# Performance work log

Hardware: AMD Instinct MI355X
Metric: run time of the kernel (lower is better)

The kernel has to match this reference:

```python
import jax, jax.numpy as jnp
import numpy as np

NEG_SLOPE = 0.2
EPS = 1e-16

def gat_layer(x, W, a_src, a_dst, bias, src, dst, N, H, C):
    # x: [N, F_in]; W: [F_in, H*C]; a_src/a_dst: [H, C]; bias: [H*C]
    h = (x @ W).reshape(N, H, C)                       # [N,H,C]
    alpha_src = (h * a_src[None]).sum(-1)              # [N,H]
    alpha_dst = (h * a_dst[None]).sum(-1)              # [N,H]
    e = jax.nn.leaky_relu(alpha_src[src] + alpha_dst[dst], NEG_SLOPE)  # [E,H]
    m = jax.ops.segment_max(e, dst, num_segments=N)    # [N,H]
    ex = jnp.exp(e - m[dst])
    s = jax.ops.segment_sum(ex, dst, num_segments=N)   # [N,H]
    alpha = ex / (s[dst] + EPS)                        # [E,H]
    out = jax.ops.segment_sum(h[src] * alpha[:, :, None], dst, num_segments=N)  # [N,H,C]
    return out.reshape(N, H * C) + bias

def setup_inputs() -> dict:
    key = jax.random.key(0)
    ks = jax.random.split(key, 12)
    N, E, Ep = 50000, 800000, 100000
    Fin, Hd, Co, H = 128, 128, 64, 2
    x = jax.random.normal(ks[0], (N, Fin), jnp.float32)
    edge_index = jax.random.randint(ks[1], (2, E), 0, N, jnp.int64)
    pos_edge_index = jax.random.randint(ks[2], (2, Ep), 0, N, jnp.int64)
    W1 = jax.random.normal(ks[3], (Fin, H * Hd), jnp.float32) / np.sqrt(Fin)
    a1_src = jax.random.normal(ks[4], (H, Hd), jnp.float32) / np.sqrt(Hd)
    a1_dst = jax.random.normal(ks[5], (H, Hd), jnp.float32) / np.sqrt(Hd)
    b1 = jnp.zeros((H * Hd,), jnp.float32)
    W2 = jax.random.normal(ks[6], (H * Hd, H * Co), jnp.float32) / np.sqrt(H * Hd)
    a2_src = jax.random.normal(ks[7], (H, Co), jnp.float32) / np.sqrt(Co)
    a2_dst = jax.random.normal(ks[8], (H, Co), jnp.float32) / np.sqrt(Co)
    b2 = jnp.zeros((H * Co,), jnp.float32)
    return {"x": x, "edge_index": edge_index, "pos_edge_index": pos_edge_index,
            "W1": W1, "a1_src": a1_src, "a1_dst": a1_dst, "b1": b1,
            "W2": W2, "a2_src": a2_src, "a2_dst": a2_dst, "b2": b2}

def reference(x, edge_index, pos_edge_index, W1, a1_src, a1_dst, b1, W2, a2_src, a2_dst, b2):
    N = x.shape[0]
    H = a1_src.shape[0]
    # add self loops (PyG GATConv default)
    loop = jnp.arange(N, dtype=edge_index.dtype)
    src = jnp.concatenate([edge_index[0], loop])
    dst = jnp.concatenate([edge_index[1], loop])
    h1 = gat_layer(x, W1, a1_src, a1_dst, b1, src, dst, N, H, a1_src.shape[1])
    h1 = jax.nn.relu(h1)  # dropout is identity in eval mode
    z = gat_layer(h1, W2, a2_src, a2_dst, b2, src, dst, N, H, a2_src.shape[1])
    # decode: dot product per positive edge
    return (z[pos_edge_index[0]] * z[pos_edge_index[1]]).sum(-1)
```

## Files before the change

### kernel.cpp

```cpp
#include <hip/hip_runtime.h>

#define NEG_SLOPE 0.2f
#define EPS_F 1e-16f
#define STILE 4096

typedef short short8 __attribute__((ext_vector_type(8)));
typedef float f32x4 __attribute__((ext_vector_type(4)));

__device__ __forceinline__ unsigned short f2bf(float x) {
    unsigned u = __float_as_uint(x);
    return (unsigned short)((u + 0x7FFFu + ((u >> 16) & 1u)) >> 16);
}
__device__ __forceinline__ float bflo(unsigned q) { return __uint_as_float(q << 16); }
__device__ __forceinline__ float bfhi(unsigned q) { return __uint_as_float(q & 0xFFFF0000u); }


template<int MB, int K, typename TIN>
__device__ __forceinline__ void gemm_body(
        const TIN* __restrict__ X, const unsigned short* __restrict__ Wt,
        unsigned short* __restrict__ Y, float* __restrict__ as_out,
        float* __restrict__ ad_out, const float* __restrict__ a_srcf,
        const float* __restrict__ a_dstf, int N, int bid,
        unsigned short* lds) {
    constexpr int NT_ = MB / 16;
    constexpr int C   = MB / 2;
    constexpr int KS  = K / 32;
    constexpr int KP  = K + 8;
    int tid  = threadIdx.x;
    int w    = tid >> 6, lane = tid & 63;
    int li   = lane & 15, kc = lane >> 4;
    int n0   = bid * 64 + w * 16;
    int arow = min(n0 + li, N - 1);

    constexpr int CHUNKS = MB * K / 8;
#pragma unroll
    for (int c = 0; c < CHUNKS / 256; ++c) {
        int id = tid + c * 256;
        int m = id / (K / 8), k8 = id % (K / 8);
        *(uint4*)&lds[m * KP + k8 * 8] = *(const uint4*)&Wt[m * K + k8 * 8];
    }
    short8 a[KS];
#pragma unroll
    for (int ks = 0; ks < KS; ++ks) {
        if constexpr (sizeof(TIN) == 4) {
            const float* xp = (const float*)X + (size_t)arow * K + ks * 32 + kc * 8;
            float4 xa = *(const float4*)xp;
            float4 xb = *(const float4*)(xp + 4);
            a[ks][0] = (short)f2bf(xa.x); a[ks][1] = (short)f2bf(xa.y);
            a[ks][2] = (short)f2bf(xa.z); a[ks][3] = (short)f2bf(xa.w);
            a[ks][4] = (short)f2bf(xb.x); a[ks][5] = (short)f2bf(xb.y);
            a[ks][6] = (short)f2bf(xb.z); a[ks][7] = (short)f2bf(xb.w);
        } else {
            a[ks] = *(const short8*)((const unsigned short*)X + (size_t)arow * K + ks * 32 + kc * 8);
        }
    }
    __syncthreads();

    f32x4 acc[NT_];
#pragma unroll
    for (int ct = 0; ct < NT_; ++ct) acc[ct] = (f32x4){0.f, 0.f, 0.f, 0.f};
#pragma unroll
    for (int ct = 0; ct < NT_; ++ct) {
        const unsigned short* wb = lds + (ct * 16 + li) * KP + kc * 8;
#pragma unroll
        for (int ks = 0; ks < KS; ++ks) {
            short8 b = *(const short8*)(wb + ks * 32);
            acc[ct] = __builtin_amdgcn_mfma_f32_16x16x32_bf16(a[ks], b, acc[ct], 0, 0, 0);
        }
    }

    float av[NT_], dv[NT_];
#pragma unroll
    for (int ct = 0; ct < NT_; ++ct) {
        av[ct] = a_srcf[ct * 16 + li];
        dv[ct] = a_dstf[ct * 16 + li];
    }
    int row_base = n0 + kc * 4;
#pragma unroll
    for (int r = 0; r < 4; ++r) {
        int n = row_base + r;
        float vs0 = 0.f, vs1 = 0.f, vd0 = 0.f, vd1 = 0.f;
#pragma unroll
        for (int ct = 0; ct < NT_; ++ct) {
            float v = acc[ct][r];
            if (ct * 16 < C) { vs0 = fmaf(v, av[ct], vs0); vd0 = fmaf(v, dv[ct], vd0); }
            else             { vs1 = fmaf(v, av[ct], vs1); vd1 = fmaf(v, dv[ct], vd1); }
        }
#pragma unroll
        for (int off = 1; off < 16; off <<= 1) {
            vs0 += __shfl_xor(vs0, off);
            vs1 += __shfl_xor(vs1, off);
            vd0 += __shfl_xor(vd0, off);
            vd1 += __shfl_xor(vd1, off);
        }
        if (n < N) {
            if (li == 0) {
                as_out[n * 2] = vs0; as_out[n * 2 + 1] = vs1;
                ad_out[n * 2] = vd0; ad_out[n * 2 + 1] = vd1;
            }
#pragma unroll
            for (int ct = 0; ct < NT_; ++ct)
                Y[(size_t)n * MB + ct * 16 + li] = f2bf(acc[ct][r]);
        }
    }
}

__device__ __forceinline__ void scan_part_body(const int* __restrict__ deg,
                                               int* __restrict__ tsum, int b) {
    __shared__ int wsh[4];
    int t = threadIdx.x;
    int base = b * STILE + t * 16;
    int sum = 0;
#pragma unroll
    for (int j = 0; j < 16; j += 4) {
        int4 q = *(const int4*)&deg[base + j];
        sum += q.x + q.y + q.z + q.w;
    }
#pragma unroll
    for (int off = 32; off; off >>= 1) sum += __shfl_down(sum, off);
    if ((t & 63) == 0) wsh[t >> 6] = sum;
    __syncthreads();
    if (t == 0) tsum[b] = wsh[0] + wsh[1] + wsh[2] + wsh[3];
}


__global__ void k_prep_hist(const float* __restrict__ W1, unsigned short* __restrict__ Wt1,
                            int K1, int M1,
                            const float* __restrict__ W2, unsigned short* __restrict__ Wt2,
                            int K2, int M2, int nPrepBlk,
                            const int* __restrict__ ei, int E, int N,
                            int* __restrict__ deg) {
    if ((int)blockIdx.x < nPrepBlk) {
        int i = blockIdx.x * 256 + threadIdx.x;
        int n1 = M1 * K1;
        if (i < n1) {
            int m = i / K1, k = i - m * K1;
            Wt1[i] = f2bf(W1[(size_t)k * M1 + m]);
        } else {
            int j = i - n1;
            if (j < M2 * K2) {
                int m = j / K2, k = j - m * K2;
                Wt2[j] = f2bf(W2[(size_t)k * M2 + m]);
            }
        }
    } else {
        int e = (blockIdx.x - nPrepBlk) * 256 + threadIdx.x;
        if (e >= E + N) return;
        int d = (e < E) ? ei[E + e] : e - E;
        atomicAdd(&deg[d], 1);
    }
}

__global__ __launch_bounds__(256) void k_gemm1_scan(
        const float* __restrict__ X, const unsigned short* __restrict__ Wt,
        unsigned short* __restrict__ Y, float* __restrict__ as_out,
        float* __restrict__ ad_out, const float* __restrict__ a_srcf,
        const float* __restrict__ a_dstf, int N, int GB,
        const int* __restrict__ deg, int* __restrict__ tsum) {
    __shared__ __align__(16) unsigned short lds[256 * (128 + 8)];
    if ((int)blockIdx.x < GB)
        gemm_body<256, 128, float>(X, Wt, Y, as_out, ad_out, a_srcf, a_dstf, N,
                                   blockIdx.x, lds);
    else
        scan_part_body(deg, tsum, blockIdx.x - GB);
}

__global__ __launch_bounds__(256) void k_gemm2(
        const unsigned short* __restrict__ X, const unsigned short* __restrict__ Wt,
        unsigned short* __restrict__ Y, float* __restrict__ as_out,
        float* __restrict__ ad_out, const float* __restrict__ a_srcf,
        const float* __restrict__ a_dstf, int N) {
    __shared__ __align__(16) unsigned short lds[128 * (256 + 8)];
    gemm_body<128, 256, unsigned short>(X, Wt, Y, as_out, ad_out, a_srcf, a_dstf, N,
                                        blockIdx.x, lds);
}

__global__ __launch_bounds__(256) void scan_final(const int* __restrict__ deg,
                                                  const int* __restrict__ tsum,
                                                  int* __restrict__ rowptr,
                                                  int* __restrict__ cursor) {
    int b = blockIdx.x, t = threadIdx.x, lane = t & 63, wid = t >> 6;
    int base = b * STILE + t * 16;
    int tpre = 0;
    for (int j = 0; j < b; ++j) tpre += tsum[j];
    int v[16];
    int sum = 0;
#pragma unroll
    for (int j = 0; j < 16; j += 4) {
        int4 q = *(const int4*)&deg[base + j];
        v[j] = q.x; v[j + 1] = q.y; v[j + 2] = q.z; v[j + 3] = q.w;
        sum += q.x + q.y + q.z + q.w;
    }
    int x = sum;
#pragma unroll
    for (int off = 1; off < 64; off <<= 1) {
        int y = __shfl_up(x, off);
        if (lane >= off) x += y;
    }
    __shared__ int wtot[4];
    if (lane == 63) wtot[wid] = x;
    __syncthreads();
    int woff = 0;
    for (int wi = 0; wi < wid; ++wi) woff += wtot[wi];
    int run = tpre + woff + (x - sum);
    int outv[16];
#pragma unroll
    for (int j = 0; j < 16; ++j) { outv[j] = run; run += v[j]; }
#pragma unroll
    for (int j = 0; j < 16; j += 4) {
        *(int4*)&rowptr[base + j] = make_int4(outv[j], outv[j+1], outv[j+2], outv[j+3]);
        *(int4*)&cursor[base + j] = make_int4(0, 0, 0, 0);
    }
}

__global__ void fill_kernel(const int* __restrict__ ei, int E, int N,
                            const int* __restrict__ rowptr, int* __restrict__ cursor,
                            int* __restrict__ csr_src) {
    int e = blockIdx.x * blockDim.x + threadIdx.x;
    if (e >= E + N) return;
    int s, d;
    if (e < E) { s = ei[e]; d = ei[E + e]; } else { s = d = e - E; }
    int pos = atomicAdd(&cursor[d], 1);
    csr_src[rowptr[d] + pos] = s;
}

template<int M, int C, typename TOUT>
__global__ __launch_bounds__(256) void fused_attn_agg(
        const int* __restrict__ rowptr, const int* __restrict__ csr_src,
        const float* __restrict__ as_, const float* __restrict__ ad_,
        const unsigned short* __restrict__ hfeat, const float* __restrict__ bias,
        TOUT* __restrict__ outp, int N, int do_relu) {
    constexpr int VEC = M / 64;
    __shared__ __align__(16) uint2 pb0[4][64];
    __shared__ __align__(16) uint2 pb1[4][64];
    int n    = (blockIdx.x * blockDim.x + threadIdx.x) >> 6;
    int lane = threadIdx.x & 63;
    int w    = (threadIdx.x >> 6) & 3;
    if (n >= N) return;
    int cbase = lane * VEC;
    int hh    = cbase / C;
    int r0 = rowptr[n], r1 = rowptr[n + 1];
    const float2* as2 = (const float2*)as_;
    float2 adv = ((const float2*)ad_)[n];
    float sa0 = 0.f, sa1 = 0.f;
    float acc[VEC];
#pragma unroll
    for (int v = 0; v < VEC; ++v) acc[v] = 0.f;
    const uint2* ap = (hh == 0) ? pb0[w] : pb1[w];

    for (int base = r0; base < r1; base += 64) {
        int cnt = min(64, r1 - base);
        int srcl = 0;
        float sc0 = -INFINITY, sc1 = -INFINITY;
        if (lane < cnt) {
            srcl = csr_src[base + lane];
            float2 asv = as2[srcl];
            float e0 = asv.x + adv.x;
            float e1 = asv.y + adv.y;
            sc0 = (e0 > 0.f) ? e0 : NEG_SLOPE * e0;
            sc1 = (e1 > 0.f) ? e1 : NEG_SLOPE * e1;
        }
        float p0 = expf(sc0), p1 = expf(sc1);
        sa0 += p0; sa1 += p1;
        unsigned off = (unsigned)srcl * (M * 2);
        pb0[w][lane] = make_uint2(off, __float_as_uint(p0));
        pb1[w][lane] = make_uint2(off, __float_as_uint(p1));
        for (int e = 0; e < cnt; e += 2) {
            uint4 qq = *(const uint4*)&ap[e];
            float pa = __uint_as_float(qq.y);
            float pc = __uint_as_float(qq.w);
            const unsigned short* hp0 = (const unsigned short*)((const char*)hfeat + qq.x) + cbase;
            const unsigned short* hp1 = (const unsigned short*)((const char*)hfeat + qq.z) + cbase;
            if constexpr (VEC == 4) {
                uint2 g0 = *(const uint2*)hp0;
                uint2 g1 = *(const uint2*)hp1;
                acc[0] += pa * bflo(g0.x); acc[1] += pa * bfhi(g0.x);
                acc[2] += pa * bflo(g0.y); acc[3] += pa * bfhi(g0.y);
                acc[0] += pc * bflo(g1.x); acc[1] += pc * bfhi(g1.x);
                acc[2] += pc * bflo(g1.y); acc[3] += pc * bfhi(g1.y);
            } else {
                unsigned g0 = *(const unsigned*)hp0;
                unsigned g1 = *(const unsigned*)hp1;
                acc[0] += pa * bflo(g0); acc[1] += pa * bfhi(g0);
                acc[0] += pc * bflo(g1); acc[1] += pc * bfhi(g1);
            }
        }
    }
#pragma unroll
    for (int off = 32; off; off >>= 1) {
        sa0 += __shfl_xor(sa0, off);
        sa1 += __shfl_xor(sa1, off);
    }
    float ssum = (hh == 0) ? sa0 : sa1;
    float inv = 1.f / (ssum + EPS_F);
    float o[VEC];
#pragma unroll
    for (int v = 0; v < VEC; ++v) {
        float val = acc[v] * inv + bias[cbase + v];
        o[v] = do_relu ? fmaxf(val, 0.f) : val;
    }
    if constexpr (sizeof(TOUT) == 2) {
        unsigned short* op = (unsigned short*)outp + (size_t)n * M + cbase;
        if constexpr (VEC == 4) {
            uint2 pk;
            pk.x = (unsigned)f2bf(o[0]) | ((unsigned)f2bf(o[1]) << 16);
            pk.y = (unsigned)f2bf(o[2]) | ((unsigned)f2bf(o[3]) << 16);
            *(uint2*)op = pk;
        } else {
            *(unsigned*)op = (unsigned)f2bf(o[0]) | ((unsigned)f2bf(o[1]) << 16);
        }
    } else {
        float* op = (float*)outp + (size_t)n * M + cbase;
        if constexpr (VEC == 4) *(float4*)op = make_float4(o[0], o[1], o[2], o[3]);
        else                    *(float2*)op = make_float2(o[0], o[1]);
    }
}

__global__ void decode_kernel(const int* __restrict__ pei, int Ep,
                              const float* __restrict__ z, int D,
                              float* __restrict__ out) {
    int wid  = (blockIdx.x * blockDim.x + threadIdx.x) >> 6;
    int lane = threadIdx.x & 63;
    if (wid >= Ep) return;
    int a = pei[wid], b = pei[Ep + wid];
    const float2* za = (const float2*)(z + (size_t)a * D);
    const float2* zb = (const float2*)(z + (size_t)b * D);
    float s = 0.f;
    for (int i = lane; i < D / 2; i += 64) {
        float2 xv = za[i], yv = zb[i];
        s += xv.x * yv.x + xv.y * yv.y;
    }
    for (int off = 32; off; off >>= 1) s += __shfl_down(s, off);
    if (lane == 0) out[wid] = s;
}

extern "C" void kernel_launch(void* const* d_in, const int* in_sizes, int n_in,
                              void* d_out, int out_size, void* d_ws, size_t ws_size,
                              hipStream_t stream) {
    const float* x   = (const float*)d_in[0];
    const int*   ei  = (const int*)d_in[1];
    const int*   pei = (const int*)d_in[2];
    const float* W1  = (const float*)d_in[3];
    const float* a1s = (const float*)d_in[4];
    const float* a1d = (const float*)d_in[5];
    const float* b1  = (const float*)d_in[6];
    const float* W2  = (const float*)d_in[7];
    const float* a2s = (const float*)d_in[8];
    const float* a2d = (const float*)d_in[9];
    const float* b2  = (const float*)d_in[10];
    float* out = (float*)d_out;

    const int M1  = in_sizes[6];
    const int Fin = in_sizes[3] / M1;
    const int N   = in_sizes[0] / Fin;
    const int E   = in_sizes[1] / 2;
    const int Ep  = in_sizes[2] / 2;
    const int M2  = in_sizes[10];
    const int Etot = E + N;
    const int NT  = (N + STILE - 1) / STILE;

    unsigned short* hbf  = (unsigned short*)d_ws;
    unsigned short* h1bf = hbf + (size_t)N * M1;
    float* zbuf    = (float*)(h1bf + (size_t)N * M1);
    float* as_     = zbuf + (size_t)N * M2;
    float* ad_     = as_ + (size_t)N * 2;
    int*   deg     = (int*)(ad_ + (size_t)N * 2);
    int*   rowptr  = deg + (size_t)NT * STILE;
    int*   cursor  = rowptr + (size_t)NT * STILE;
    int*   tsum    = cursor + (size_t)NT * STILE;
    int*   csr_src = tsum + 64;
    unsigned short* wt1 = (unsigned short*)(csr_src + Etot);
    unsigned short* wt2 = wt1 + (size_t)M1 * Fin;

    dim3 blk256(256);

    hipMemsetAsync(deg, 0, (size_t)NT * STILE * sizeof(int), stream);

    int nPrepBlk = (M1 * Fin + M2 * M1 + 255) / 256;
    int nHistBlk = (Etot + 255) / 256;
    k_prep_hist<<<nPrepBlk + nHistBlk, blk256, 0, stream>>>(
        W1, wt1, Fin, M1, W2, wt2, M1, M2, nPrepBlk, ei, E, N, deg);

    int GB = (N + 63) / 64;
    k_gemm1_scan<<<GB + NT, blk256, 0, stream>>>(
        x, wt1, hbf, as_, ad_, a1s, a1d, N, GB, deg, tsum);

    scan_final<<<NT, blk256, 0, stream>>>(deg, tsum, rowptr, cursor);
    fill_kernel<<<nHistBlk, blk256, 0, stream>>>(ei, E, N, rowptr, cursor, csr_src);

    fused_attn_agg<256, 128, unsigned short><<<(N + 3) / 4, blk256, 0, stream>>>(
        rowptr, csr_src, as_, ad_, hbf, b1, h1bf, N, 1);

    k_gemm2<<<(N + 63) / 64, blk256, 0, stream>>>(
        h1bf, wt2, hbf, as_, ad_, a2s, a2d, N);

    fused_attn_agg<128, 64, float><<<(N + 3) / 4, blk256, 0, stream>>>(
        rowptr, csr_src, as_, ad_, hbf, b2, zbuf, N, 0);

    decode_kernel<<<(Ep * 64 + 255) / 256, blk256, 0, stream>>>(
        pei, Ep, zbuf, M2, out);
}
```

Measured before the change: 254.5 us.

## Fuse CSR fill into gemm1, store z as bf16, halve decode wave work

Moves the scan before the first GEMM so the CSR fill can run as extra blocks in the same launch as gemm1, overlapping atomic scatter with matrix work. The layer-2 output z is now stored in bf16, and decode processes two edges per wavefront with 32 lanes each, reading packed bf16 pairs. Hidden-feature pointer arithmetic in the aggregation loop is simplified by hoisting the column offset. The bf16 z adds rounding error to the final dot products, and the scan kernels now run as standalone small launches.

```diff
diff --git a/kernel.cpp b/kernel.cpp
--- a/kernel.cpp
+++ b/kernel.cpp
@@ -121,6 +121,18 @@
     if ((t & 63) == 0) wsh[t >> 6] = sum;
     __syncthreads();
     if (t == 0) tsum[b] = wsh[0] + wsh[1] + wsh[2] + wsh[3];
+}
+
+__device__ __forceinline__ void fill_body(const int* __restrict__ ei, int E, int N,
+                                          const int* __restrict__ rowptr,
+                                          int* __restrict__ cursor,
+                                          int* __restrict__ csr_src, int bid) {
+    int e = bid * 256 + threadIdx.x;
+    if (e >= E + N) return;
+    int s, d;
+    if (e < E) { s = ei[e]; d = ei[E + e]; } else { s = d = e - E; }
+    int pos = atomicAdd(&cursor[d], 1);
+    csr_src[rowptr[d] + pos] = s;
 }
 
 
@@ -151,28 +163,9 @@
     }
 }
 
-__global__ __launch_bounds__(256) void k_gemm1_scan(
-        const float* __restrict__ X, const unsigned short* __restrict__ Wt,
-        unsigned short* __restrict__ Y, float* __restrict__ as_out,
-        float* __restrict__ ad_out, const float* __restrict__ a_srcf,
-        const float* __restrict__ a_dstf, int N, int GB,
-        const int* __restrict__ deg, int* __restrict__ tsum) {
-    __shared__ __align__(16) unsigned short lds[256 * (128 + 8)];
-    if ((int)blockIdx.x < GB)
-        gemm_body<256, 128, float>(X, Wt, Y, as_out, ad_out, a_srcf, a_dstf, N,
-                                   blockIdx.x, lds);
-    else
-        scan_part_body(deg, tsum, blockIdx.x - GB);
-}
-
-__global__ __launch_bounds__(256) void k_gemm2(
-        const unsigned short* __restrict__ X, const unsigned short* __restrict__ Wt,
-        unsigned short* __restrict__ Y, float* __restrict__ as_out,
-        float* __restrict__ ad_out, const float* __restrict__ a_srcf,
-        const float* __restrict__ a_dstf, int N) {
-    __shared__ __align__(16) unsigned short lds[128 * (256 + 8)];
-    gemm_body<128, 256, unsigned short>(X, Wt, Y, as_out, ad_out, a_srcf, a_dstf, N,
-                                        blockIdx.x, lds);
+__global__ __launch_bounds__(256) void k_scan_part(const int* __restrict__ deg,
+                                                   int* __restrict__ tsum) {
+    scan_part_body(deg, tsum, blockIdx.x);
 }
 
 __global__ __launch_bounds__(256) void scan_final(const int* __restrict__ deg,
@@ -213,15 +206,30 @@
     }
 }
 
-__global__ void fill_kernel(const int* __restrict__ ei, int E, int N,
-                            const int* __restrict__ rowptr, int* __restrict__ cursor,
-                            int* __restrict__ csr_src) {
-    int e = blockIdx.x * blockDim.x + threadIdx.x;
-    if (e >= E + N) return;
-    int s, d;
-    if (e < E) { s = ei[e]; d = ei[E + e]; } else { s = d = e - E; }
-    int pos = atomicAdd(&cursor[d], 1);
-    csr_src[rowptr[d] + pos] = s;
+__global__ __launch_bounds__(256) void k_gemm1_fill(
+        const float* __restrict__ X, const unsigned short* __restrict__ Wt,
+        unsigned short* __restrict__ Y, float* __restrict__ as_out,
+        float* __restrict__ ad_out, const float* __restrict__ a_srcf,
+        const float* __restrict__ a_dstf, int N, int GB,
+        const int* __restrict__ ei, int E,
+        const int* __restrict__ rowptr, int* __restrict__ cursor,
+        int* __restrict__ csr_src) {
+    __shared__ __align__(16) unsigned short lds[256 * (128 + 8)];
+    if ((int)blockIdx.x < GB)
+        gemm_body<256, 128, float>(X, Wt, Y, as_out, ad_out, a_srcf, a_dstf, N,
+                                   blockIdx.x, lds);
+    else
+        fill_body(ei, E, N, rowptr, cursor, csr_src, blockIdx.x - GB);
+}
+
+__global__ __launch_bounds__(256) void k_gemm2(
+        const unsigned short* __restrict__ X, const unsigned short* __restrict__ Wt,
+        unsigned short* __restrict__ Y, float* __restrict__ as_out,
+        float* __restrict__ ad_out, const float* __restrict__ a_srcf,
+        const float* __restrict__ a_dstf, int N) {
+    __shared__ __align__(16) unsigned short lds[128 * (256 + 8)];
+    gemm_body<128, 256, unsigned short>(X, Wt, Y, as_out, ad_out, a_srcf, a_dstf, N,
+                                        blockIdx.x, lds);
 }
 
 template<int M, int C, typename TOUT>
@@ -247,6 +255,7 @@
 #pragma unroll
     for (int v = 0; v < VEC; ++v) acc[v] = 0.f;
     const uint2* ap = (hh == 0) ? pb0[w] : pb1[w];
+    const char* hbc = (const char*)hfeat + (size_t)cbase * 2;
 
     for (int base = r0; base < r1; base += 64) {
         int cnt = min(64, r1 - base);
@@ -269,8 +278,8 @@
             uint4 qq = *(const uint4*)&ap[e];
             float pa = __uint_as_float(qq.y);
             float pc = __uint_as_float(qq.w);
-            const unsigned short* hp0 = (const unsigned short*)((const char*)hfeat + qq.x) + cbase;
-            const unsigned short* hp1 = (const unsigned short*)((const char*)hfeat + qq.z) + cbase;
+            const char* hp0 = hbc + qq.x;
+            const char* hp1 = hbc + qq.z;
             if constexpr (VEC == 4) {
                 uint2 g0 = *(const uint2*)hp0;
                 uint2 g1 = *(const uint2*)hp1;
@@ -317,21 +326,21 @@
 }
 
 __global__ void decode_kernel(const int* __restrict__ pei, int Ep,
-                              const float* __restrict__ z, int D,
+                              const unsigned short* __restrict__ z, int D,
                               float* __restrict__ out) {
-    int wid  = (blockIdx.x * blockDim.x + threadIdx.x) >> 6;
+    int wv   = (blockIdx.x * blockDim.x + threadIdx.x) >> 6;
     int lane = threadIdx.x & 63;
-    if (wid >= Ep) return;
-    int a = pei[wid], b = pei[Ep + wid];
-    const float2* za = (const float2*)(z + (size_t)a * D);
-    const float2* zb = (const float2*)(z + (size_t)b * D);
-    float s = 0.f;
-    for (int i = lane; i < D / 2; i += 64) {
-        float2 xv = za[i], yv = zb[i];
-        s += xv.x * yv.x + xv.y * yv.y;
-    }
-    for (int off = 32; off; off >>= 1) s += __shfl_down(s, off);
-    if (lane == 0) out[wid] = s;
+    int half = lane >> 5, sl = lane & 31;
+    int e  = wv * 2 + half;
+    int ec = min(e, Ep - 1);
+    int a = pei[ec], b = pei[Ep + ec];
+    uint2 qa = *(const uint2*)(z + (size_t)a * D + sl * 4);
+    uint2 qb = *(const uint2*)(z + (size_t)b * D + sl * 4);
+    float s = bflo(qa.x) * bflo(qb.x) + bfhi(qa.x) * bfhi(qb.x)
+            + bflo(qa.y) * bflo(qb.y) + bfhi(qa.y) * bfhi(qb.y);
+#pragma unroll
+    for (int off = 16; off; off >>= 1) s += __shfl_xor(s, off);
+    if (sl == 0 && e < Ep) out[e] = s;
 }
 
 extern "C" void kernel_launch(void* const* d_in, const int* in_sizes, int n_in,
@@ -361,8 +370,8 @@
 
     unsigned short* hbf  = (unsigned short*)d_ws;
     unsigned short* h1bf = hbf + (size_t)N * M1;
-    float* zbuf    = (float*)(h1bf + (size_t)N * M1);
-    float* as_     = zbuf + (size_t)N * M2;
+    unsigned short* zbf  = h1bf + (size_t)N * M1;
+    float* as_     = (float*)(zbf + (size_t)N * M2);
     float* ad_     = as_ + (size_t)N * 2;
     int*   deg     = (int*)(ad_ + (size_t)N * 2);
     int*   rowptr  = deg + (size_t)NT * STILE;
@@ -381,12 +390,13 @@
     k_prep_hist<<<nPrepBlk + nHistBlk, blk256, 0, stream>>>(
         W1, wt1, Fin, M1, W2, wt2, M1, M2, nPrepBlk, ei, E, N, deg);
 
+    k_scan_part<<<NT, blk256, 0, stream>>>(deg, tsum);
+    scan_final<<<NT, blk256, 0, stream>>>(deg, tsum, rowptr, cursor);
+
     int GB = (N + 63) / 64;
-    k_gemm1_scan<<<GB + NT, blk256, 0, stream>>>(
-        x, wt1, hbf, as_, ad_, a1s, a1d, N, GB, deg, tsum);
-
-    scan_final<<<NT, blk256, 0, stream>>>(deg, tsum, rowptr, cursor);
-    fill_kernel<<<nHistBlk, blk256, 0, stream>>>(ei, E, N, rowptr, cursor, csr_src);
+    k_gemm1_fill<<<GB + nHistBlk, blk256, 0, stream>>>(
+        x, wt1, hbf, as_, ad_, a1s, a1d, N, GB,
+        ei, E, rowptr, cursor, csr_src);
 
     fused_attn_agg<256, 128, unsigned short><<<(N + 3) / 4, blk256, 0, stream>>>(
         rowptr, csr_src, as_, ad_, hbf, b1, h1bf, N, 1);
@@ -394,9 +404,12 @@
     k_gemm2<<<(N + 63) / 64, blk256, 0, stream>>>(
         h1bf, wt2, hbf, as_, ad_, a2s, a2d, N);
 
-    fused_attn_agg<128, 64, float><<<(N + 3) / 4, blk256, 0, stream>>>(
-        rowptr, csr_src, as_, ad_, hbf, b2, zbuf, N, 0);
-
-    decode_kernel<<<(Ep * 64 + 255) / 256, blk256, 0, stream>>>(
-        pei, Ep, zbuf, M2, out);
-}
+    fused_attn_agg<128, 64, unsigned short><<<(N + 3) / 4, blk256, 0, stream>>>(
+        rowptr, csr_src, as_, ad_, hbf, b2, zbf, N, 0);
+
+    {
+        int waves = (Ep + 1) / 2;
+        decode_kernel<<<(waves * 64 + 255) / 256, blk256, 0, stream>>>(
+            pei, Ep, zbf, M2, out);
+    }
+}
```

Result: faster. 239.2 us (-6.0%).
